# Kernel tuning notes

Measured on AMD Instinct MI355X. Metric: run time of the kernel, lower is better.

Reference implementation:

```python
import jax, jax.numpy as jnp
import numpy as np

NEG = -1e30  # log-space 'zero' (safe substitute for -inf)
EPS = 1e-7   # keras.backend.epsilon(), used by ctc_batch_cost


def _ctc_forward(logp, z, allow2):
    """CTC negative log-likelihood via the forward DP in log space.
    logp:   [B, T, C] log-probabilities
    z:      [B, S] extended label sequence (blanks interleaved), S = 2L+1
    allow2: [B, S] bool, whether the skip transition (s-2 -> s) is legal
    Returns [B, 1] loss (matches keras ctc_batch_cost output shape).
    """
    B, T, C = logp.shape
    S = z.shape[1]
    # Gather per-timestep log-probs of extended labels: [B, T, S] -> [T, B, S]
    b_idx = jnp.arange(B)[:, None, None]
    t_idx = jnp.arange(T)[None, :, None]
    lp_z = jnp.transpose(logp[b_idx, t_idx, z[:, None, :]], (1, 0, 2))

    s_idx = jnp.arange(S)[None, :]
    alpha0 = jnp.where(s_idx < 2, lp_z[0], NEG)  # paths may start at blank or first label

    def step(alpha, lp_t):
        a1 = jnp.concatenate([jnp.full((B, 1), NEG, alpha.dtype), alpha[:, :-1]], axis=1)
        a2 = jnp.concatenate([jnp.full((B, 2), NEG, alpha.dtype), alpha[:, :-2]], axis=1)
        a2 = jnp.where(allow2, a2, NEG)
        m = jnp.maximum(alpha, jnp.maximum(a1, a2))
        lse = m + jnp.log(jnp.exp(alpha - m) + jnp.exp(a1 - m) + jnp.exp(a2 - m))
        return lp_t + lse, None

    alphaT, _ = jax.lax.scan(step, alpha0, lp_z[1:])
    # Paths end at last blank (S-1) or last label (S-2)
    last, last2 = alphaT[:, -1], alphaT[:, -2]
    m = jnp.maximum(last, last2)
    ll = m + jnp.log(jnp.exp(last - m) + jnp.exp(last2 - m))
    return -ll[:, None]


def setup_inputs() -> dict:
    key = jax.random.key(0)
    k1, k2 = jax.random.split(key)
    B, T, C, L = 32, 2048, 256, 256
    # ctc_batch_cost expects post-softmax probabilities
    y_pred = jax.nn.softmax(jax.random.normal(k1, (B, T, C), jnp.float32), axis=-1)
    y_true = jax.random.randint(k2, (B, L), 0, C - 1)  # blank = C-1 excluded from labels
    return {"y_true": y_true, "y_pred": y_pred}


def reference(y_true, y_pred):
    B, T, C = y_pred.shape
    blank = C - 1
    L = y_true.shape[1]
    S = 2 * L + 1
    labels = y_true.astype(jnp.int32)
    # Extended label sequence: blank, l0, blank, l1, ..., blank
    z = jnp.full((B, S), blank, jnp.int32).at[:, 1::2].set(labels)
    z_m2 = jnp.concatenate([jnp.full((B, 2), -1, jnp.int32), z[:, :-2]], axis=1)
    allow2 = (z != blank) & (z != z_m2)
    logp = jnp.log(y_pred + EPS)
    return _ctc_forward(logp, z, allow2)
```

## Files before the change

### kernel.cpp

```cpp
#include <hip/hip_runtime.h>

#define TT   2048
#define CC   256
#define LL   256
#define SS   513
#define TM   1023
#define EPSF (1e-7f)
#define LN2F (0.69314718055994531f)
#define DPTH 8
#define RBTH 64
#define NCH  127
#define EMINI (-2000000000)
#define GSTR 260

#if __has_builtin(__builtin_amdgcn_frexp_expf)
#define FREXP_EXP __builtin_amdgcn_frexp_expf
#else
static __device__ __forceinline__ int FREXP_EXP(float x){ int e; return (frexpf(x,&e), e); }
#endif
#if __has_builtin(__builtin_amdgcn_ldexpf)
#define LDEXP __builtin_amdgcn_ldexpf
#else
#define LDEXP ldexpf
#endif

__launch_bounds__(256, 4)
__global__ void ctc_gather_kernel(const int* __restrict__ y_true,
                                  const float* __restrict__ y_pred,
                                  float* __restrict__ gat)
{
    const int b   = blockIdx.x;
    const int i   = threadIdx.x;
    const int col = y_true[b * LL + i];
    const float* rp = y_pred + (size_t)b * TT * CC;
    float*       gp = gat    + (size_t)b * TT * GSTR;
    const int tch = TT / gridDim.y;
    const int t0  = blockIdx.y * tch;
    #pragma unroll 4
    for (int t = t0; t < t0 + tch; ++t) {
        gp[(size_t)t * GSTR + i] = rp[(size_t)t * CC + col] + EPSF;
        if (i < 4)
            gp[(size_t)t * GSTR + 256 + i] = rp[(size_t)t * CC + (CC - 1)] + EPSF;
    }
}

template<int NSTEP>
__device__ __forceinline__ void fwd_group(float (&f)[9], int &e, bool &mm,
        const float (&kk)[8], int lane,
        float4 o0, float4 o1, float4 o2, float4 o3,
        float4 q0, float4 q1, float4 q2, float4 q3,
        float b0, float b1, float b2, float b3)
{
    float h[8];
    #pragma unroll
    for (int j = 0; j < 8; ++j) h[j] = __shfl_up(f[j], 1);
    int he = __shfl_up(e, 1);
    if (lane == 0) {
        he = e;
        #pragma unroll
        for (int j = 0; j < 8; ++j) h[j] = 0.0f;
    }
    const int E  = mm ? (e > he ? e : he) : he;
    const int dh = he - E, dn = e - E;
    float g[17];
    #pragma unroll
    for (int j = 0; j < 8; ++j) g[j] = LDEXP(h[j], dh);
    #pragma unroll
    for (int j = 0; j < 9; ++j) g[8 + j] = LDEXP(f[j], dn);
    e = E;

#define FSW(Q, O, B, LO) do {                                                 \
        const float pv[8] = {Q.x,Q.y,Q.z,Q.w,O.x,O.y,O.z,O.w};                \
        _Pragma("unroll")                                                     \
        for (int i = 16; i >= (LO); --i) {                                    \
            if (i & 1) g[i] = (g[i] + g[i-1] + g[i-2]*kk[(i-1)>>1])           \
                              * pv[(i-1)>>1];                                 \
            else       g[i] = (g[i] + g[i-1]) * (B);                          \
        }                                                                     \
    } while (0)

    if (NSTEP == 4) {
        FSW(q0,o0,b0,2); FSW(q1,o1,b1,4); FSW(q2,o2,b2,6); FSW(q3,o3,b3,8);
    } else {
        FSW(q0,o0,b0,4); FSW(q1,o1,b1,6); FSW(q2,o2,b2,8);
    }
#undef FSW

    #pragma unroll
    for (int j = 0; j < 9; ++j) f[j] = g[8 + j];
    float mx = f[0];
    #pragma unroll
    for (int j = 1; j < 9; ++j) mx = fmaxf(mx, f[j]);
    const int em = FREXP_EXP(mx);
    #pragma unroll
    for (int j = 0; j < 9; ++j) f[j] = LDEXP(f[j], -em);
    e += em;
    mm = (mx > 0.0f);
}

template<int NSTEP>
__device__ __forceinline__ void bwd_group(float (&f)[9], int &e, bool &mm,
        const float (&kk)[8], int lane,
        float4 o0, float4 o1, float4 o2, float4 o3,
        float4 q0, float4 q1, float4 q2, float4 q3,
        float b0, float b1, float b2, float b3)
{
    float h[8];
    #pragma unroll
    for (int j = 0; j < 8; ++j) h[j] = __shfl_down(f[j + 1], 1);
    int he = __shfl_down(e, 1);
    if (lane == 63) {
        he = e;
        #pragma unroll
        for (int j = 0; j < 8; ++j) h[j] = 0.0f;
    }
    const int E  = mm ? (e > he ? e : he) : he;
    const int dh = he - E, dn = e - E;
    float g[17];
    #pragma unroll
    for (int j = 0; j < 9; ++j) g[j] = LDEXP(f[j], dn);
    #pragma unroll
    for (int j = 0; j < 8; ++j) g[9 + j] = LDEXP(h[j], dh);
    e = E;

#define BSW(O, Q, B, HI) do {                                                 \
        const float pv[8] = {O.x,O.y,O.z,O.w,Q.x,Q.y,Q.z,Q.w};                \
        _Pragma("unroll")                                                     \
        for (int i = 0; i <= (HI); ++i) {                                     \
            if (i & 1) g[i] = (g[i] + g[i+1] + g[i+2]*kk[(i-1)>>1])           \
                              * pv[(i-1)>>1];                                 \
            else       g[i] = (g[i] + g[i+1]) * (B);                          \
        }                                                                     \
    } while (0)

    if (NSTEP == 4) {
        BSW(o0,q0,b0,14); BSW(o1,q1,b1,12); BSW(o2,q2,b2,10); BSW(o3,q3,b3,8);
    } else {
        BSW(o0,q0,b0,12); BSW(o1,q1,b1,10); BSW(o2,q2,b2,8);
    }
#undef BSW

    #pragma unroll
    for (int j = 0; j < 9; ++j) f[j] = g[j];
    float mx = f[0];
    #pragma unroll
    for (int j = 1; j < 9; ++j) mx = fmaxf(mx, f[j]);
    const int em = FREXP_EXP(mx);
    #pragma unroll
    for (int j = 0; j < 9; ++j) f[j] = LDEXP(f[j], -em);
    e += em;
    mm = (mx > 0.0f);
}

__launch_bounds__(128, 1)
__global__ void ctc_grp_kernel(const int* __restrict__ y_true,
                               const float* __restrict__ y_pred,
                               const float* __restrict__ gat,
                               float* __restrict__ out)
{
    __shared__ float cw[SS];
    __shared__ int   ew[64];

    const int tid   = threadIdx.x;
    const int w     = tid >> 6;
    const int lane  = tid & 63;
    const int b     = blockIdx.x;
    const int blank = CC - 1;

    const int*   lab  = y_true + b * LL;
    const float* base = y_pred + (size_t)b * TT * CC;
    const float* gLb  = gat    + (size_t)b * TT * GSTR;

    float kk[8];
    if (w == 0) {
        #pragma unroll
        for (int j = 0; j < 8; ++j) {
            const int li  = 4 * lane - 4 + j;
            const int lic = li < 0 ? 0 : li;
            const int z   = lab[lic];
            const int zm  = (li >= 1) ? lab[li - 1] : -1;
            kk[j] = (li >= 0 && z != zm) ? 1.0f : 0.0f;
        }
    } else {
        #pragma unroll
        for (int j = 0; j < 8; ++j) {
            const int li  = 4 * lane + j;
            const int lic = li > 255 ? 255 : li;
            const int z   = lab[lic];
            kk[j] = (li <= 254 && lab[li + 1] != z) ? 1.0f : 0.0f;
        }
    }

    float f[9];
    #pragma unroll
    for (int j = 0; j < 9; ++j) f[j] = 0.0f;
    int  e = 0;
    bool mm;

    if (w == 0) {
        if (lane == 0) {
            f[0] = base[blank]        + EPSF;
            f[1] = base[lab[0]]       + EPSF;
        }
        mm = (lane == 0);
    } else {
        if (lane == 63) {
            const float* rT = base + (size_t)(TT - 1) * CC;
            f[7] = rT[lab[255]] + EPSF;
            f[8] = rT[blank]    + EPSF;
        }
        mm = (lane == 63);
    }

    const int oofs = 4 * lane;
    const int qofs = (w == 0) ? (4 * lane - 4 < 0 ? 0 : 4 * lane - 4)
                              : (4 * lane + 4);
    const int bofs = 256 + (lane & 3);
    const int dstp = (w == 0) ? GSTR : -GSTR;

    float4 s0o[4], s0q[4]; float s0b[4];
    float4 s1o[4], s1q[4]; float s1b[4];

#define LOADG(SO, SQ, SB, ROWP) do {                                          \
        const float* _rp = (ROWP);                                            \
        _Pragma("unroll")                                                     \
        for (int k = 0; k < 4; ++k) {                                         \
            SO[k] = *(const float4*)(_rp + oofs);                             \
            SQ[k] = *(const float4*)(_rp + qofs);                             \
            SB[k] = _rp[bofs];                                                \
            _rp += dstp;                                                      \
        }                                                                     \
    } while (0)

    const float* grow = (w == 0) ? (gLb + (size_t)1 * GSTR)
                                 : (gLb + (size_t)2046 * GSTR);
    LOADG(s0o, s0q, s0b, grow); grow += 4 * dstp;
    LOADG(s1o, s1q, s1b, grow); grow += 4 * dstp;

#define PROC(SO, SQ, SB, NS) do {                                             \
        const float4 a0 = SO[0], a1 = SO[1], a2 = SO[2], a3 = SO[3];          \
        const float4 p0 = SQ[0], p1 = SQ[1], p2 = SQ[2], p3 = SQ[3];          \
        const float  c0 = SB[0], c1 = SB[1], c2 = SB[2], c3 = SB[3];          \
        if (NS == 4) { LOADG(SO, SQ, SB, grow); grow += 4 * dstp; }           \
        __builtin_amdgcn_sched_barrier(0);                                    \
        if (w == 0) fwd_group<NS>(f, e, mm, kk, lane,                         \
                        a0,a1,a2,a3, p0,p1,p2,p3, c0,c1,c2,c3);               \
        else        bwd_group<NS>(f, e, mm, kk, lane,                         \
                        a0,a1,a2,a3, p0,p1,p2,p3, c0,c1,c2,c3);               \
    } while (0)

    for (int c = 0; c < 127; ++c) {
        PROC(s0o, s0q, s0b, 4);
        PROC(s1o, s1q, s1b, 4);
    }
    {
        const float4 a0 = s0o[0], a1 = s0o[1], a2 = s0o[2], a3 = s0o[3];
        const float4 p0 = s0q[0], p1 = s0q[1], p2 = s0q[2], p3 = s0q[3];
        const float  c0 = s0b[0], c1 = s0b[1], c2 = s0b[2], c3 = s0b[3];
        if (w == 0) fwd_group<4>(f, e, mm, kk, lane,
                        a0,a1,a2,a3, p0,p1,p2,p3, c0,c1,c2,c3);
        else        bwd_group<4>(f, e, mm, kk, lane,
                        a0,a1,a2,a3, p0,p1,p2,p3, c0,c1,c2,c3);
    }
    {
        const float4 a0 = s1o[0], a1 = s1o[1], a2 = s1o[2], a3 = s1o[3];
        const float4 p0 = s1q[0], p1 = s1q[1], p2 = s1q[2], p3 = s1q[3];
        const float  c0 = s1b[0], c1 = s1b[1], c2 = s1b[2], c3 = s1b[3];
        if (w == 0) fwd_group<3>(f, e, mm, kk, lane,
                        a0,a1,a2,a3, p0,p1,p2,p3, c0,c1,c2,c3);
        else        bwd_group<3>(f, e, mm, kk, lane,
                        a0,a1,a2,a3, p0,p1,p2,p3, c0,c1,c2,c3);
    }
#undef PROC
#undef LOADG

    if (w == 1) {
        float d1 = __shfl_down(f[1], 1);
        int   de = __shfl_down(e, 1);
        if (lane == 63) { d1 = 0.0f; de = e; }
        int dlt = de - e;
        if (dlt >= RBTH) {
            #pragma unroll
            for (int j = 0; j < 9; ++j) f[j] = LDEXP(f[j], -dlt);
            e = de; dlt = 0;
        }
        const float bf = LDEXP(d1, dlt);
        float cb[9];
        cb[0] = f[0] + f[1];
        cb[1] = f[1] + f[2] + f[3] * kk[0];
        cb[2] = f[2] + f[3];
        cb[3] = f[3] + f[4] + f[5] * kk[1];
        cb[4] = f[4] + f[5];
        cb[5] = f[5] + f[6] + f[7] * kk[2];
        cb[6] = f[6] + f[7];
        cb[7] = f[7] + f[8] + bf   * kk[3];
        cb[8] = f[8] + bf;
        #pragma unroll
        for (int j = 0; j < 8; ++j) cw[8 * lane + j] = cb[j];
        if (lane == 63) cw[512] = cb[8];
        ew[lane] = e;
    }

    __syncthreads();

    if (w == 0) {
        float part = 0.0f;
        #pragma unroll
        for (int j = 0; j < 8; ++j) part += f[j] * cw[8 * lane + j];
        if (lane == 63) part += f[8] * cw[512];
        int   ep = (part > 0.0f) ? (e + ew[lane]) : EMINI;
        float m  = part;
        #pragma unroll
        for (int d = 1; d < 64; d <<= 1) {
            const float mo = __shfl_xor(m, d);
            const int   eo = __shfl_xor(ep, d);
            const int   E  = ep > eo ? ep : eo;
            m  = LDEXP(m, ep - E) + LDEXP(mo, eo - E);
            ep = E;
        }
        if (lane == 0)
            out[b] = -LN2F * ((float)ep + __builtin_amdgcn_logf(m));
    }
}

__launch_bounds__(128, 1)
__global__ void ctc_fb_kernel(const int* __restrict__ y_true,
                              const float* __restrict__ y_pred,
                              float* __restrict__ out)
{
    __shared__ float cw[SS];
    __shared__ int   ew[64];

    const int tid   = threadIdx.x;
    const int w     = tid >> 6;
    const int lane  = tid & 63;
    const int b     = blockIdx.x;
    const int blank = CC - 1;

    const int*   lab  = y_true + b * LL;
    const float* base = y_pred + (size_t)b * TT * CC;

    int   col[4];
    float kup[4], kdn[4];
    #pragma unroll
    for (int i = 0; i < 4; ++i) {
        const int li = 4 * lane + i;
        const int z  = lab[li];
        col[i] = z;
        const int zm = (li >= 1) ? lab[li - 1] : -1;
        kup[i] = (z != zm) ? 1.0f : 0.0f;
        kdn[i] = (li <= 254 && lab[li + 1] != z) ? 1.0f : 0.0f;
    }

    float f[9];
    #pragma unroll
    for (int j = 0; j < 9; ++j) f[j] = 0.0f;
    int  e = 0;
    bool lzero;

    if (w == 0) {
        if (lane == 0) { f[0] = base[blank] + EPSF; f[1] = base[col[0]] + EPSF; }
        lzero = (lane != 0);
    } else {
        if (lane == 63) {
            const float* rT = base + (size_t)(TT - 1) * CC;
            f[7] = rT[col[3]] + EPSF; f[8] = rT[blank] + EPSF;
        }
        lzero = (lane != 63);
    }

    float pfb[DPTH]; float pfl[DPTH][4];
    #pragma unroll
    for (int k = 0; k < DPTH; ++k) {
        const int r = (w == 0) ? (1 + k) : (TT - 2 - k);
        const float* rp = base + (size_t)r * CC;
        pfb[k] = rp[blank];
        #pragma unroll
        for (int i = 0; i < 4; ++i) pfl[k][i] = rp[col[i]];
    }

    auto renorm = [&]() {
        float m = fmaxf(fmaxf(fmaxf(f[0], f[1]), fmaxf(f[2], f[3])),
                        fmaxf(fmaxf(f[4], f[5]), fmaxf(f[6], fmaxf(f[7], f[8]))));
        const int em = FREXP_EXP(m);
        #pragma unroll
        for (int j = 0; j < 9; ++j) f[j] = LDEXP(f[j], -em);
        e += em;
    };
    auto fwd_step = [&](float pb, float p0, float p1, float p2, float p3) {
        float u7 = __shfl_up(f[7], 1);
        int   ue = __shfl_up(e, 1);
        if (lane == 0) { u7 = 0.0f; ue = e; }
        int dlt = ue - e;
        const bool rb = lzero || (dlt >= RBTH);
        if (__ballot(rb)) {
            const int sh = rb ? -dlt : 0;
            #pragma unroll
            for (int j = 0; j < 9; ++j) f[j] = LDEXP(f[j], sh);
            e = rb ? ue : e; dlt = rb ? 0 : dlt;
            lzero = lzero && (u7 == 0.0f);
        }
        const float bf = LDEXP(u7, dlt);
        const float n0 = (f[0] + bf) * pb;
        const float n1 = (f[1] + f[0] + bf   * kup[0]) * p0;
        const float n2 = (f[2] + f[1]) * pb;
        const float n3 = (f[3] + f[2] + f[1] * kup[1]) * p1;
        const float n4 = (f[4] + f[3]) * pb;
        const float n5 = (f[5] + f[4] + f[3] * kup[2]) * p2;
        const float n6 = (f[6] + f[5]) * pb;
        const float n7 = (f[7] + f[6] + f[5] * kup[3]) * p3;
        const float n8 = (f[8] + f[7]) * pb;
        f[0]=n0; f[1]=n1; f[2]=n2; f[3]=n3; f[4]=n4;
        f[5]=n5; f[6]=n6; f[7]=n7; f[8]=n8;
    };
    auto bwd_step = [&](float pb, float p0, float p1, float p2, float p3) {
        float d1 = __shfl_down(f[1], 1);
        int   de = __shfl_down(e, 1);
        if (lane == 63) { d1 = 0.0f; de = e; }
        int dlt = de - e;
        const bool rb = lzero || (dlt >= RBTH);
        if (__ballot(rb)) {
            const int sh = rb ? -dlt : 0;
            #pragma unroll
            for (int j = 0; j < 9; ++j) f[j] = LDEXP(f[j], sh);
            e = rb ? de : e; dlt = rb ? 0 : dlt;
            lzero = lzero && (d1 == 0.0f);
        }
        const float bf = LDEXP(d1, dlt);
        const float n0 = (f[0] + f[1]) * pb;
        const float n1 = (f[1] + f[2] + f[3] * kdn[0]) * p0;
        const float n2 = (f[2] + f[3]) * pb;
        const float n3 = (f[3] + f[4] + f[5] * kdn[1]) * p1;
        const float n4 = (f[4] + f[5]) * pb;
        const float n5 = (f[5] + f[6] + f[7] * kdn[2]) * p2;
        const float n6 = (f[6] + f[7]) * pb;
        const float n7 = (f[7] + f[8] + bf   * kdn[3]) * p3;
        const float n8 = (f[8] + bf) * pb;
        f[0]=n0; f[1]=n1; f[2]=n2; f[3]=n3; f[4]=n4;
        f[5]=n5; f[6]=n6; f[7]=n7; f[8]=n8;
    };

    if (w == 0) {
        for (int c = 0; c < NCH; ++c) {
            #pragma unroll
            for (int k = 0; k < DPTH; ++k) {
                const float pb = pfb[k] + EPSF;
                const float p0 = pfl[k][0] + EPSF, p1 = pfl[k][1] + EPSF;
                const float p2 = pfl[k][2] + EPSF, p3 = pfl[k][3] + EPSF;
                int tp = 1 + c * DPTH + k + DPTH; if (tp > TM) tp = TM;
                const float* rp = base + (size_t)tp * CC;
                pfb[k] = rp[blank];
                #pragma unroll
                for (int i = 0; i < 4; ++i) pfl[k][i] = rp[col[i]];
                fwd_step(pb, p0, p1, p2, p3);
                if (k == 3 || k == 7) renorm();
            }
        }
        #pragma unroll
        for (int k = 0; k < 7; ++k) {
            fwd_step(pfb[k] + EPSF, pfl[k][0] + EPSF, pfl[k][1] + EPSF,
                     pfl[k][2] + EPSF, pfl[k][3] + EPSF);
            if (k == 3) renorm();
        }
    } else {
        for (int c = 0; c < NCH; ++c) {
            #pragma unroll
            for (int k = 0; k < DPTH; ++k) {
                const float pb = pfb[k] + EPSF;
                const float p0 = pfl[k][0] + EPSF, p1 = pfl[k][1] + EPSF;
                const float p2 = pfl[k][2] + EPSF, p3 = pfl[k][3] + EPSF;
                int tp = (TT - 2) - (c * DPTH + k) - DPTH; if (tp < TM + 1) tp = TM + 1;
                const float* rp = base + (size_t)tp * CC;
                pfb[k] = rp[blank];
                #pragma unroll
                for (int i = 0; i < 4; ++i) pfl[k][i] = rp[col[i]];
                bwd_step(pb, p0, p1, p2, p3);
                if (k == 3 || k == 7) renorm();
            }
        }
        #pragma unroll
        for (int k = 0; k < 7; ++k) {
            bwd_step(pfb[k] + EPSF, pfl[k][0] + EPSF, pfl[k][1] + EPSF,
                     pfl[k][2] + EPSF, pfl[k][3] + EPSF);
            if (k == 3) renorm();
        }

        float d1 = __shfl_down(f[1], 1);
        int   de = __shfl_down(e, 1);
        if (lane == 63) { d1 = 0.0f; de = e; }
        int dlt = de - e;
        if (dlt >= RBTH) {
            #pragma unroll
            for (int j = 0; j < 9; ++j) f[j] = LDEXP(f[j], -dlt);
            e = de; dlt = 0;
        }
        const float bf = LDEXP(d1, dlt);
        float cb[9];
        cb[0] = f[0] + f[1];
        cb[1] = f[1] + f[2] + f[3] * kdn[0];
        cb[2] = f[2] + f[3];
        cb[3] = f[3] + f[4] + f[5] * kdn[1];
        cb[4] = f[4] + f[5];
        cb[5] = f[5] + f[6] + f[7] * kdn[2];
        cb[6] = f[6] + f[7];
        cb[7] = f[7] + f[8] + bf   * kdn[3];
        cb[8] = f[8] + bf;
        #pragma unroll
        for (int j = 0; j < 8; ++j) cw[8 * lane + j] = cb[j];
        if (lane == 63) cw[512] = cb[8];
        ew[lane] = e;
    }

    __syncthreads();

    if (w == 0) {
        float part = 0.0f;
        #pragma unroll
        for (int j = 0; j < 8; ++j) part += f[j] * cw[8 * lane + j];
        if (lane == 63) part += f[8] * cw[512];
        int   ep = (part > 0.0f) ? (e + ew[lane]) : EMINI;
        float m  = part;
        #pragma unroll
        for (int d = 1; d < 64; d <<= 1) {
            const float mo = __shfl_xor(m, d);
            const int   eo = __shfl_xor(ep, d);
            const int   E  = ep > eo ? ep : eo;
            m  = LDEXP(m, ep - E) + LDEXP(mo, eo - E);
            ep = E;
        }
        if (lane == 0)
            out[b] = -LN2F * ((float)ep + __builtin_amdgcn_logf(m));
    }
}

extern "C" void kernel_launch(void* const* d_in, const int* in_sizes, int n_in,
                              void* d_out, int out_size, void* d_ws, size_t ws_size,
                              hipStream_t stream)
{
    const int*   y_true = (const int*)d_in[0];
    const float* y_pred = (const float*)d_in[1];
    float*       out    = (float*)d_out;
    const int B = in_sizes[0] / LL;

    const size_t need = (size_t)B * TT * GSTR * sizeof(float);
    if (ws_size >= need) {
        float* gat = (float*)d_ws;
        ctc_gather_kernel<<<dim3(B, 32), 256, 0, stream>>>(y_true, y_pred, gat);
        ctc_grp_kernel<<<B, 128, 0, stream>>>(y_true, y_pred, gat, out);
    } else {
        ctc_fb_kernel<<<B, 128, 0, stream>>>(y_true, y_pred, out);
    }
}
```

Before: 175.4 us.

## Interleave forward and backward CTC recursions in a single wavefront

Replaces the two-wave block, where one wave ran the forward recursion and the other the backward recursion, with a single 64-lane wave that runs both chains interleaved. The final combination then happens in registers with no shared memory and no block barrier. The intent is to hide each chain's dependent-latency with independent work from the other chain and to skip the LDS exchange. In exchange, each lane carries double the register state and load buffers, and each SIMD runs only one wave per batch, which could serialize issue.

Measured after the change: 276.8 us. +57.8%, slower.

```diff
diff --git a/kernel.cpp b/kernel.cpp
--- a/kernel.cpp
+++ b/kernel.cpp
@@ -152,18 +152,13 @@
     mm = (mx > 0.0f);
 }
 
-__launch_bounds__(128, 1)
-__global__ void ctc_grp_kernel(const int* __restrict__ y_true,
-                               const float* __restrict__ y_pred,
-                               const float* __restrict__ gat,
-                               float* __restrict__ out)
+__launch_bounds__(64, 1)
+__global__ void ctc_dual_kernel(const int* __restrict__ y_true,
+                                const float* __restrict__ y_pred,
+                                const float* __restrict__ gat,
+                                float* __restrict__ out)
 {
-    __shared__ float cw[SS];
-    __shared__ int   ew[64];
-
-    const int tid   = threadIdx.x;
-    const int w     = tid >> 6;
-    const int lane  = tid & 63;
+    const int lane  = threadIdx.x;
     const int b     = blockIdx.x;
     const int blank = CC - 1;
 
@@ -171,156 +166,130 @@
     const float* base = y_pred + (size_t)b * TT * CC;
     const float* gLb  = gat    + (size_t)b * TT * GSTR;
 
-    float kk[8];
-    if (w == 0) {
-        #pragma unroll
-        for (int j = 0; j < 8; ++j) {
-            const int li  = 4 * lane - 4 + j;
+    float kkf[8], kkb[8];
+    #pragma unroll
+    for (int j = 0; j < 8; ++j) {
+        {   const int li  = 4 * lane - 4 + j;
             const int lic = li < 0 ? 0 : li;
             const int z   = lab[lic];
             const int zm  = (li >= 1) ? lab[li - 1] : -1;
-            kk[j] = (li >= 0 && z != zm) ? 1.0f : 0.0f;
-        }
-    } else {
-        #pragma unroll
-        for (int j = 0; j < 8; ++j) {
-            const int li  = 4 * lane + j;
+            kkf[j] = (li >= 0 && z != zm) ? 1.0f : 0.0f; }
+        {   const int li  = 4 * lane + j;
             const int lic = li > 255 ? 255 : li;
             const int z   = lab[lic];
-            kk[j] = (li <= 254 && lab[li + 1] != z) ? 1.0f : 0.0f;
-        }
-    }
-
-    float f[9];
-    #pragma unroll
-    for (int j = 0; j < 9; ++j) f[j] = 0.0f;
-    int  e = 0;
-    bool mm;
-
-    if (w == 0) {
-        if (lane == 0) {
-            f[0] = base[blank]        + EPSF;
-            f[1] = base[lab[0]]       + EPSF;
-        }
-        mm = (lane == 0);
-    } else {
-        if (lane == 63) {
-            const float* rT = base + (size_t)(TT - 1) * CC;
-            f[7] = rT[lab[255]] + EPSF;
-            f[8] = rT[blank]    + EPSF;
-        }
-        mm = (lane == 63);
-    }
-
-    const int oofs = 4 * lane;
-    const int qofs = (w == 0) ? (4 * lane - 4 < 0 ? 0 : 4 * lane - 4)
-                              : (4 * lane + 4);
-    const int bofs = 256 + (lane & 3);
-    const int dstp = (w == 0) ? GSTR : -GSTR;
-
-    float4 s0o[4], s0q[4]; float s0b[4];
-    float4 s1o[4], s1q[4]; float s1b[4];
-
-#define LOADG(SO, SQ, SB, ROWP) do {                                          \
-        const float* _rp = (ROWP);                                            \
+            kkb[j] = (li <= 254 && lab[li + 1] != z) ? 1.0f : 0.0f; }
+    }
+
+    float ff[9], fb[9];
+    #pragma unroll
+    for (int j = 0; j < 9; ++j) { ff[j] = 0.0f; fb[j] = 0.0f; }
+    int  ef = 0, eb = 0;
+    bool mmf, mmb;
+
+    if (lane == 0) {
+        ff[0] = base[blank]  + EPSF;
+        ff[1] = base[lab[0]] + EPSF;
+    }
+    mmf = (lane == 0);
+    if (lane == 63) {
+        const float* rT = base + (size_t)(TT - 1) * CC;
+        fb[7] = rT[lab[255]] + EPSF;
+        fb[8] = rT[blank]    + EPSF;
+    }
+    mmb = (lane == 63);
+
+    const int oofs  = 4 * lane;
+    const int qofsF = (4 * lane - 4 < 0) ? 0 : (4 * lane - 4);
+    const int qofsB = 4 * lane + 4;
+    const int bofs  = 256 + (lane & 3);
+
+    float4 fAo[4], fAq[4]; float fAb[4];
+    float4 fBo[4], fBq[4]; float fBb[4];
+    float4 bAo[4], bAq[4]; float bAb[4];
+    float4 bBo[4], bBq[4]; float bBb[4];
+
+#define LOADF(SO, SQ, SB, RP) do {                                            \
         _Pragma("unroll")                                                     \
         for (int k = 0; k < 4; ++k) {                                         \
-            SO[k] = *(const float4*)(_rp + oofs);                             \
-            SQ[k] = *(const float4*)(_rp + qofs);                             \
-            SB[k] = _rp[bofs];                                                \
-            _rp += dstp;                                                      \
-        }                                                                     \
-    } while (0)
-
-    const float* grow = (w == 0) ? (gLb + (size_t)1 * GSTR)
-                                 : (gLb + (size_t)2046 * GSTR);
-    LOADG(s0o, s0q, s0b, grow); grow += 4 * dstp;
-    LOADG(s1o, s1q, s1b, grow); grow += 4 * dstp;
-
-#define PROC(SO, SQ, SB, NS) do {                                             \
-        const float4 a0 = SO[0], a1 = SO[1], a2 = SO[2], a3 = SO[3];          \
-        const float4 p0 = SQ[0], p1 = SQ[1], p2 = SQ[2], p3 = SQ[3];          \
-        const float  c0 = SB[0], c1 = SB[1], c2 = SB[2], c3 = SB[3];          \
-        if (NS == 4) { LOADG(SO, SQ, SB, grow); grow += 4 * dstp; }           \
-        __builtin_amdgcn_sched_barrier(0);                                    \
-        if (w == 0) fwd_group<NS>(f, e, mm, kk, lane,                         \
-                        a0,a1,a2,a3, p0,p1,p2,p3, c0,c1,c2,c3);               \
-        else        bwd_group<NS>(f, e, mm, kk, lane,                         \
-                        a0,a1,a2,a3, p0,p1,p2,p3, c0,c1,c2,c3);               \
-    } while (0)
+            SO[k] = *(const float4*)((RP) + k * GSTR + oofs);                 \
+            SQ[k] = *(const float4*)((RP) + k * GSTR + qofsF);                \
+            SB[k] = (RP)[k * GSTR + bofs];                                    \
+        } } while (0)
+#define LOADB(SO, SQ, SB, RP) do {                                            \
+        _Pragma("unroll")                                                     \
+        for (int k = 0; k < 4; ++k) {                                         \
+            SO[k] = *(const float4*)((RP) - k * GSTR + oofs);                 \
+            SQ[k] = *(const float4*)((RP) - k * GSTR + qofsB);                \
+            SB[k] = (RP)[-k * GSTR + bofs];                                   \
+        } } while (0)
+
+#define FGRP(S, NS) fwd_group<NS>(ff, ef, mmf, kkf, lane,                     \
+        S##o[0],S##o[1],S##o[2],S##o[3], S##q[0],S##q[1],S##q[2],S##q[3],     \
+        S##b[0],S##b[1],S##b[2],S##b[3])
+#define BGRP(S, NS) bwd_group<NS>(fb, eb, mmb, kkb, lane,                     \
+        S##o[0],S##o[1],S##o[2],S##o[3], S##q[0],S##q[1],S##q[2],S##q[3],     \
+        S##b[0],S##b[1],S##b[2],S##b[3])
+
+    const float* pF = gLb + (size_t)1 * GSTR;
+    const float* pB = gLb + (size_t)2046 * GSTR;
+    LOADF(fAo, fAq, fAb, pF); pF += 4 * GSTR;
+    LOADB(bAo, bAq, bAb, pB); pB -= 4 * GSTR;
+    LOADF(fBo, fBq, fBb, pF); pF += 4 * GSTR;
+    LOADB(bBo, bBq, bBb, pB); pB -= 4 * GSTR;
 
     for (int c = 0; c < 127; ++c) {
-        PROC(s0o, s0q, s0b, 4);
-        PROC(s1o, s1q, s1b, 4);
-    }
-    {
-        const float4 a0 = s0o[0], a1 = s0o[1], a2 = s0o[2], a3 = s0o[3];
-        const float4 p0 = s0q[0], p1 = s0q[1], p2 = s0q[2], p3 = s0q[3];
-        const float  c0 = s0b[0], c1 = s0b[1], c2 = s0b[2], c3 = s0b[3];
-        if (w == 0) fwd_group<4>(f, e, mm, kk, lane,
-                        a0,a1,a2,a3, p0,p1,p2,p3, c0,c1,c2,c3);
-        else        bwd_group<4>(f, e, mm, kk, lane,
-                        a0,a1,a2,a3, p0,p1,p2,p3, c0,c1,c2,c3);
-    }
-    {
-        const float4 a0 = s1o[0], a1 = s1o[1], a2 = s1o[2], a3 = s1o[3];
-        const float4 p0 = s1q[0], p1 = s1q[1], p2 = s1q[2], p3 = s1q[3];
-        const float  c0 = s1b[0], c1 = s1b[1], c2 = s1b[2], c3 = s1b[3];
-        if (w == 0) fwd_group<3>(f, e, mm, kk, lane,
-                        a0,a1,a2,a3, p0,p1,p2,p3, c0,c1,c2,c3);
-        else        bwd_group<3>(f, e, mm, kk, lane,
-                        a0,a1,a2,a3, p0,p1,p2,p3, c0,c1,c2,c3);
-    }
-#undef PROC
-#undef LOADG
-
-    if (w == 1) {
-        float d1 = __shfl_down(f[1], 1);
-        int   de = __shfl_down(e, 1);
-        if (lane == 63) { d1 = 0.0f; de = e; }
-        int dlt = de - e;
-        if (dlt >= RBTH) {
-            #pragma unroll
-            for (int j = 0; j < 9; ++j) f[j] = LDEXP(f[j], -dlt);
-            e = de; dlt = 0;
-        }
-        const float bf = LDEXP(d1, dlt);
-        float cb[9];
-        cb[0] = f[0] + f[1];
-        cb[1] = f[1] + f[2] + f[3] * kk[0];
-        cb[2] = f[2] + f[3];
-        cb[3] = f[3] + f[4] + f[5] * kk[1];
-        cb[4] = f[4] + f[5];
-        cb[5] = f[5] + f[6] + f[7] * kk[2];
-        cb[6] = f[6] + f[7];
-        cb[7] = f[7] + f[8] + bf   * kk[3];
-        cb[8] = f[8] + bf;
-        #pragma unroll
-        for (int j = 0; j < 8; ++j) cw[8 * lane + j] = cb[j];
-        if (lane == 63) cw[512] = cb[8];
-        ew[lane] = e;
-    }
-
-    __syncthreads();
-
-    if (w == 0) {
-        float part = 0.0f;
-        #pragma unroll
-        for (int j = 0; j < 8; ++j) part += f[j] * cw[8 * lane + j];
-        if (lane == 63) part += f[8] * cw[512];
-        int   ep = (part > 0.0f) ? (e + ew[lane]) : EMINI;
-        float m  = part;
-        #pragma unroll
-        for (int d = 1; d < 64; d <<= 1) {
-            const float mo = __shfl_xor(m, d);
-            const int   eo = __shfl_xor(ep, d);
-            const int   E  = ep > eo ? ep : eo;
-            m  = LDEXP(m, ep - E) + LDEXP(mo, eo - E);
-            ep = E;
-        }
-        if (lane == 0)
-            out[b] = -LN2F * ((float)ep + __builtin_amdgcn_logf(m));
-    }
+        FGRP(fA, 4); BGRP(bA, 4);
+        LOADF(fAo, fAq, fAb, pF); pF += 4 * GSTR;
+        LOADB(bAo, bAq, bAb, pB); pB -= 4 * GSTR;
+        FGRP(fB, 4); BGRP(bB, 4);
+        LOADF(fBo, fBq, fBb, pF); pF += 4 * GSTR;
+        LOADB(bBo, bBq, bBb, pB); pB -= 4 * GSTR;
+    }
+    FGRP(fA, 4); BGRP(bA, 4);
+    FGRP(fB, 3); BGRP(bB, 3);
+
+#undef LOADF
+#undef LOADB
+#undef FGRP
+#undef BGRP
+
+    float d1 = __shfl_down(fb[1], 1);
+    int   de = __shfl_down(eb, 1);
+    if (lane == 63) { d1 = 0.0f; de = eb; }
+    int dlt = de - eb;
+    if (dlt >= RBTH) {
+        #pragma unroll
+        for (int j = 0; j < 9; ++j) fb[j] = LDEXP(fb[j], -dlt);
+        eb = de; dlt = 0;
+    }
+    const float bf = LDEXP(d1, dlt);
+    float cb[9];
+    cb[0] = fb[0] + fb[1];
+    cb[1] = fb[1] + fb[2] + fb[3] * kkb[0];
+    cb[2] = fb[2] + fb[3];
+    cb[3] = fb[3] + fb[4] + fb[5] * kkb[1];
+    cb[4] = fb[4] + fb[5];
+    cb[5] = fb[5] + fb[6] + fb[7] * kkb[2];
+    cb[6] = fb[6] + fb[7];
+    cb[7] = fb[7] + fb[8] + bf    * kkb[3];
+    cb[8] = fb[8] + bf;
+
+    float part = 0.0f;
+    #pragma unroll
+    for (int j = 0; j < 8; ++j) part += ff[j] * cb[j];
+    if (lane == 63) part += ff[8] * cb[8];
+    int   ep = (part > 0.0f) ? (ef + eb) : EMINI;
+    float m  = part;
+    #pragma unroll
+    for (int d = 1; d < 64; d <<= 1) {
+        const float mo = __shfl_xor(m, d);
+        const int   eo = __shfl_xor(ep, d);
+        const int   E  = ep > eo ? ep : eo;
+        m  = LDEXP(m, ep - E) + LDEXP(mo, eo - E);
+        ep = E;
+    }
+    if (lane == 0)
+        out[b] = -LN2F * ((float)ep + __builtin_amdgcn_logf(m));
 }
 
 __launch_bounds__(128, 1)
@@ -546,7 +515,7 @@
     if (ws_size >= need) {
         float* gat = (float*)d_ws;
         ctc_gather_kernel<<<dim3(B, 32), 256, 0, stream>>>(y_true, y_pred, gat);
-        ctc_grp_kernel<<<B, 128, 0, stream>>>(y_true, y_pred, gat, out);
+        ctc_dual_kernel<<<B, 64, 0, stream>>>(y_true, y_pred, gat, out);
     } else {
         ctc_fb_kernel<<<B, 128, 0, stream>>>(y_true, y_pred, out);
     }
```
